# Kernel optimization log

Measured on AMD Instinct MI355X. Metric: run time of the kernel, lower is better.

The kernel has to match this reference:

```python
import jax, jax.numpy as jnp
import numpy as np

B, N, D_MODEL, N_HEADS, WINDOW = 2, 2048, 1024, 16, 512
HEAD_DIM = D_MODEL // N_HEADS

def setup_inputs() -> dict:
    key = jax.random.key(0)
    k1, k2, k3 = jax.random.split(key, 3)
    x = jax.random.normal(k1, (B, N, D_MODEL), dtype=jnp.float32)
    W_qkv = jax.random.normal(k2, (D_MODEL, 3 * D_MODEL), dtype=jnp.float32) * 0.02
    W_proj = jax.random.normal(k3, (D_MODEL, D_MODEL), dtype=jnp.float32) * 0.02
    b_proj = jnp.zeros((D_MODEL,), dtype=jnp.float32)
    return {"x": x, "W_qkv": W_qkv, "W_proj": W_proj, "b_proj": b_proj}

def reference(x, W_qkv, W_proj, b_proj):
    Bx, Nx, C = x.shape
    H, Dh = N_HEADS, C // N_HEADS
    scale = Dh ** -0.5
    window = min(WINDOW, Nx)
    half = window // 2
    # qkv: [B,N,3C] -> [3,B,H,N,Dh]
    qkv = (x @ W_qkv).reshape(Bx, Nx, 3, H, Dh).transpose(2, 0, 3, 1, 4)
    q, k, v = qkv[0], qkv[1], qkv[2]
    # banded mask: allowed iff i-half <= j <= i+half
    i = jnp.arange(Nx)[:, None]
    j = jnp.arange(Nx)[None, :]
    allowed = jnp.abs(i - j) <= half  # [N,N] bool
    attn = jnp.einsum('bhqd,bhkd->bhqk', q, k) * scale
    attn = jnp.where(allowed[None, None], attn, -jnp.inf)
    attn = jax.nn.softmax(attn, axis=-1)
    out = jnp.einsum('bhqk,bhkd->bhqd', attn, v)
    out = out.transpose(0, 2, 1, 3).reshape(Bx, Nx, C)
    return out @ W_proj + b_proj
```

## Files before the change

kernel.cpp:

```cpp
#include <hip/hip_runtime.h>
#include <stdint.h>


typedef _Float16 f16x8 __attribute__((ext_vector_type(8)));
typedef _Float16 f16x4 __attribute__((ext_vector_type(4)));
typedef __fp16   fp16x2n __attribute__((ext_vector_type(2)));
typedef float    f32x2 __attribute__((ext_vector_type(2)));
typedef float    f32x4 __attribute__((ext_vector_type(4)));
typedef float    f32x16 __attribute__((ext_vector_type(16)));

#define MFMA16(a, b, c) __builtin_amdgcn_mfma_f32_16x16x32_f16((a), (b), (c), 0, 0, 0)
#define MFMA32(a, b, c) __builtin_amdgcn_mfma_f32_32x32x16_f16((a), (b), (c), 0, 0, 0)

__device__ __forceinline__ void gload16(const void* g, void* l) {
  __builtin_amdgcn_global_load_lds(
      (const __attribute__((address_space(1))) void*)g,
      (__attribute__((address_space(3))) void*)l, 16, 0, 0);
}

__device__ __forceinline__ unsigned pk2(float a, float b) {
  fp16x2n t = __builtin_amdgcn_cvt_pkrtz(a, b);
  return __builtin_bit_cast(unsigned, t);
}

__global__ __launch_bounds__(256) void prep(const float* __restrict__ x,
                                            const float* __restrict__ wqkv,
                                            const float* __restrict__ wproj,
                                            _Float16* __restrict__ Xb,
                                            _Float16* __restrict__ Wqt,
                                            _Float16* __restrict__ Wpt) {
  __shared__ float t[64][65];
  const int id = blockIdx.x, tid = threadIdx.x;
  if (id < 4096) {
    int i = (id * 256 + tid) * 4;
    float4 v = *(const float4*)(x + i);
    f16x4 h;
    h[0] = (_Float16)v.x; h[1] = (_Float16)v.y;
    h[2] = (_Float16)v.z; h[3] = (_Float16)v.w;
    *(f16x4*)(Xb + i) = h;
    return;
  }
  const float* in; _Float16* out; int N, bx, by;
  if (id < 4864) { int tt = id - 4096; in = wqkv; out = Wqt; N = 3072; bx = tt % 48; by = tt / 48; }
  else           { int tt = id - 4864; in = wproj; out = Wpt; N = 1024; bx = tt & 15; by = tt >> 4; }
  const int n0 = bx * 64, k0 = by * 64;
  {
    int j = tid & 63;
#pragma unroll
    for (int p = 0; p < 16; p++) {
      int i = p * 4 + (tid >> 6);
      t[i][j] = in[(size_t)(k0 + i) * N + n0 + j];
    }
  }
  __syncthreads();
  {
    int i = tid & 63;
#pragma unroll
    for (int p = 0; p < 16; p++) {
      int j = p * 4 + (tid >> 6);
      out[(size_t)(n0 + j) * 1024 + k0 + i] = (_Float16)t[i][j];
    }
  }
}

__global__ __launch_bounds__(256) void vtrans(const _Float16* __restrict__ V,
                                              _Float16* __restrict__ Vt) {
  __shared__ _Float16 t[64][66];
  const int tid = threadIdx.x;
  const int bh = blockIdx.y, n0 = blockIdx.x * 64;
  const _Float16* Vg = V + (size_t)bh * 131072;
  {
    int dh0 = (tid & 7) * 8;
#pragma unroll
    for (int p = 0; p < 2; p++) {
      int nl = p * 32 + (tid >> 3);
      f16x8 v = *(const f16x8*)(Vg + (size_t)(n0 + nl) * 64 + dh0);
#pragma unroll
      for (int e = 0; e < 8; e++) t[nl][dh0 + e] = v[e];
    }
  }
  __syncthreads();
  {
    int dh = tid >> 2, nb = (tid & 3) * 16;
    f16x8 a, b;
#pragma unroll
    for (int e = 0; e < 8; e++) { a[e] = t[nb + e][dh]; b[e] = t[nb + 8 + e][dh]; }
    _Float16* dst = Vt + (size_t)bh * 131072 + (size_t)dh * 2048 + n0 + nb;
    *(f16x8*)dst = a;
    *(f16x8*)(dst + 8) = b;
  }
}

template <int BM, int BN, int EPI>
__global__ __launch_bounds__(256) void gemm16(const _Float16* __restrict__ A,
                                              const _Float16* __restrict__ Bt,
                                              const int K,
                                              _Float16* __restrict__ oh,
                                              float* __restrict__ of,
                                              const float* __restrict__ bias,
                                              const int Nout) {
  constexpr int RF = BM / 32, CF = BN / 32;
  constexpr int SLABS = (BM + BN) / 8;
  __shared__ __align__(16) char smem[(BM + BN) * 128];
  char* As = smem;
  char* Bs = smem + BM * 128;
  const int tid = threadIdx.x, wave = tid >> 6, lane = tid & 63;
  const int il = lane & 15, ih = lane >> 4;
  const int bm = blockIdx.y * BM, bn = blockIdx.x * BN;
  const int wm = wave >> 1, wn = wave & 1;
  const int rs = lane >> 3, cp = lane & 7;

  f32x4 acc[RF][CF] = {};

  for (int k0 = 0; k0 < K; k0 += 64) {
    __syncthreads();
#pragma unroll
    for (int s0 = 0; s0 < SLABS / 4; s0++) {
      int s = wave + s0 * 4;
      int row = s * 8 + rs;
      int c = cp ^ (row & 7);
      if (row < BM)
        gload16(A + (size_t)(bm + row) * K + k0 + c * 8, As + s * 1024);
      else
        gload16(Bt + (size_t)(bn + row - BM) * K + k0 + c * 8, smem + s * 1024);
    }
    __syncthreads();
#pragma unroll
    for (int ks = 0; ks < 2; ks++) {
      f16x8 af[RF], bf[CF];
#pragma unroll
      for (int rf = 0; rf < RF; rf++) {
        int R = wm * (BM / 2) + rf * 16 + il;
        af[rf] = *(const f16x8*)(As + R * 128 + (((ks * 4 + ih) ^ (R & 7)) * 16));
      }
#pragma unroll
      for (int cf = 0; cf < CF; cf++) {
        int C = wn * (BN / 2) + cf * 16 + il;
        bf[cf] = *(const f16x8*)(Bs + C * 128 + (((ks * 4 + ih) ^ (C & 7)) * 16));
      }
#pragma unroll
      for (int rf = 0; rf < RF; rf++)
#pragma unroll
        for (int cf = 0; cf < CF; cf++)
          acc[rf][cf] = MFMA16(af[rf], bf[cf], acc[rf][cf]);
    }
  }

#pragma unroll
  for (int rf = 0; rf < RF; rf++)
#pragma unroll
    for (int cf = 0; cf < CF; cf++)
#pragma unroll
      for (int r = 0; r < 4; r++) {
        int row = bm + wm * (BM / 2) + rf * 16 + ih * 4 + r;
        int col = bn + wn * (BN / 2) + cf * 16 + il;
        float v = acc[rf][cf][r];
        if (EPI == 0) {
          int sec = col >> 10, cc = col & 1023;
          if (sec == 0) v *= 0.18033688f;
          size_t plane = (size_t)(sec * 32 + (row >> 11) * 16 + (cc >> 6));
          oh[plane * 131072 + (size_t)(row & 2047) * 64 + (cc & 63)] = (_Float16)v;
        } else {
          of[(size_t)row * Nout + col] = v + bias[col];
        }
      }
}

__global__ __launch_bounds__(512) void attn(const _Float16* __restrict__ QKV,
                                            const _Float16* __restrict__ VT,
                                            _Float16* __restrict__ O2) {
  __shared__ __align__(16) char smem[51200];
  const int tid = threadIdx.x, wave = tid >> 6, lane = tid & 63;
  const int qw = wave >> 1, sh = wave & 1;
  const int cl = lane & 31, hl = lane >> 5;
  const int rs = lane >> 3, cp = lane & 7;
  const int q0 = blockIdx.x * 128, bh = blockIdx.y;
  const _Float16* Qg = QKV + (size_t)bh * 131072;
  const _Float16* Kg = QKV + 4194304 + (size_t)bh * 131072;
  const _Float16* Vg = VT + (size_t)bh * 131072;
  const int t0 = (q0 >= 256) ? q0 - 256 : 0;
  const int t1 = (q0 + 384 <= 2048) ? q0 + 384 : 2048;
  const int niter = (t1 - t0) >> 6;

#pragma unroll
  for (int q = 0; q < 2; q++) {
    int s = 2 * wave + q;
    int row = s * 8 + rs;
    int c = cp ^ (row & 7);
    gload16(Qg + (size_t)(q0 + row) * 64 + c * 8, smem + s * 1024);
  }
  {
    char* B0 = smem + 18432;
    int row = wave * 8 + rs;
    int c = cp ^ (row & 7);
    gload16(Kg + (size_t)(t0 + row) * 64 + c * 8, B0 + wave * 1024);
    gload16(Vg + (size_t)row * 2048 + t0 + c * 8, B0 + 8192 + wave * 1024);
  }
  __syncthreads();

  f16x8 bq[4];
  {
    int row = 32 * qw + cl;
#pragma unroll
    for (int ks = 0; ks < 4; ks++)
      bq[ks] = *(const f16x8*)(smem + row * 128 + (((ks * 2 + hl) ^ (row & 7)) * 16));
  }
  __syncthreads();

  char* Pw = smem + wave * 2304;
  f32x16 oacc[2] = {};
  float l_acc = 0.f;
  const int a0 = q0 + 32 * qw;

  for (int i = 0; i < niter; i++) {
    const int kt = t0 + i * 64;
    char* Bc = smem + 18432 + (i & 1) * 16384;
    if (i + 1 < niter) {
      char* Bn = smem + 18432 + ((i + 1) & 1) * 16384;
      int row = wave * 8 + rs;
      int c = cp ^ (row & 7);
      gload16(Kg + (size_t)(kt + 64 + row) * 64 + c * 8, Bn + wave * 1024);
      gload16(Vg + (size_t)row * 2048 + (kt + 64) + c * 8, Bn + 8192 + wave * 1024);
    }
    const int d0 = a0 - (kt + 32 * sh);
    if (d0 < 288 && d0 > -288) {
      char* Ksm = Bc;
      char* Vsm = Bc + 8192;
      f32x16 st = {};
      {
        const int krow = 32 * sh + cl;
#pragma unroll
        for (int ks = 0; ks < 4; ks++) {
          f16x8 ak = *(const f16x8*)(Ksm + krow * 128 + (((ks * 2 + hl) ^ (krow & 7)) * 16));
          st = MFMA32(ak, bq[ks], st);
        }
      }
#pragma unroll
      for (int g = 0; g < 4; g++) {
        float v[4];
#pragma unroll
        for (int i2 = 0; i2 < 4; i2++) {
          float e = __builtin_amdgcn_exp2f(st[4 * g + i2]);
          int kl = 8 * g + 4 * hl + i2;
          if (d0 == 256) e = (cl <= kl) ? e : 0.f;
          else if (d0 == -256) e = (cl >= kl) ? e : 0.f;
          l_acc += e;
          v[i2] = e;
        }
        uint2 w2 = {pk2(v[0], v[1]), pk2(v[2], v[3])};
        *(uint2*)(Pw + cl * 72 + 16 * g + 8 * hl) = w2;
      }
#pragma unroll
      for (int ks2 = 0; ks2 < 2; ks2++) {
        union { uint2 u2[2]; f16x8 h; } bp;
        bp.u2[0] = *(const uint2*)(Pw + cl * 72 + 32 * ks2 + 16 * hl);
        bp.u2[1] = *(const uint2*)(Pw + cl * 72 + 32 * ks2 + 16 * hl + 8);
#pragma unroll
        for (int db = 0; db < 2; db++) {
          int vrow = 32 * db + cl;
          f16x8 av = *(const f16x8*)(Vsm + vrow * 128 +
                                     (((4 * sh + 2 * ks2 + hl) ^ (vrow & 7)) * 16));
          oacc[db] = MFMA32(av, bp.h, oacc[db]);
        }
      }
    }
    __syncthreads();
  }

  const float lp = l_acc + __shfl_xor(l_acc, 32);
  char* Mq = smem + qw * 8448;
  if (sh == 1) {
#pragma unroll
    for (int db = 0; db < 2; db++)
#pragma unroll
      for (int g = 0; g < 4; g++) {
        int dh0 = 32 * db + 8 * g + 4 * hl;
        f32x2 a = {oacc[db][4 * g + 0], oacc[db][4 * g + 1]};
        f32x2 b = {oacc[db][4 * g + 2], oacc[db][4 * g + 3]};
        *(f32x2*)(Mq + cl * 264 + dh0 * 4) = a;
        *(f32x2*)(Mq + cl * 264 + dh0 * 4 + 8) = b;
      }
    if (hl == 0) *(float*)(smem + 34816 + (qw * 32 + cl) * 4) = lp;
  }
  __syncthreads();
  if (sh == 0) {
    float lo = *(const float*)(smem + 34816 + (qw * 32 + cl) * 4);
    float inv = 1.0f / (lp + lo);
    const int b = bh >> 4, h = bh & 15;
    _Float16* dst = O2 + (size_t)(b * 2048 + a0 + cl) * 1024 + h * 64;
#pragma unroll
    for (int db = 0; db < 2; db++)
#pragma unroll
      for (int g = 0; g < 4; g++) {
        int dh0 = 32 * db + 8 * g + 4 * hl;
        f32x2 a = *(const f32x2*)(Mq + cl * 264 + dh0 * 4);
        f32x2 b2 = *(const f32x2*)(Mq + cl * 264 + dh0 * 4 + 8);
        uint2 pkd = {pk2((oacc[db][4 * g + 0] + a[0]) * inv,
                         (oacc[db][4 * g + 1] + a[1]) * inv),
                     pk2((oacc[db][4 * g + 2] + b2[0]) * inv,
                         (oacc[db][4 * g + 3] + b2[1]) * inv)};
        *(uint2*)(dst + dh0) = pkd;
      }
  }
}


extern "C" void kernel_launch(void* const* d_in, const int* in_sizes, int n_in,
                              void* d_out, int out_size, void* d_ws, size_t ws_size,
                              hipStream_t stream) {
  const float* x = (const float*)d_in[0];
  const float* wqkv = (const float*)d_in[1];
  const float* wproj = (const float*)d_in[2];
  const float* bproj = (const float*)d_in[3];
  float* out = (float*)d_out;
  char* ws = (char*)d_ws;

  _Float16* Xb  = (_Float16*)(ws);
  _Float16* Wqt = (_Float16*)(ws + (size_t)(8  << 20));
  _Float16* Wpt = (_Float16*)(ws + (size_t)(14 << 20));
  _Float16* QKV = (_Float16*)(ws + (size_t)(16 << 20));
  _Float16* Vt  = (_Float16*)(ws + (size_t)(40 << 20));
  _Float16* O2  = (_Float16*)(ws);

  prep<<<5120, 256, 0, stream>>>(x, wqkv, wproj, Xb, Wqt, Wpt);
  gemm16<128, 128, 0><<<dim3(24, 32), 256, 0, stream>>>(Xb, Wqt, 1024, QKV, nullptr,
                                                        nullptr, 0);
  vtrans<<<dim3(32, 32), 256, 0, stream>>>(QKV + 8388608, Vt);
  attn<<<dim3(16, 32), 512, 0, stream>>>(QKV, Vt, O2);
  gemm16<128, 64, 1><<<dim3(16, 32), 256, 0, stream>>>(O2, Wpt, 1024, nullptr, out,
                                                       bproj, 1024);
}
```

Baseline: 160.9 us.

## Double-buffer GEMM LDS tiles with K-step 32 to overlap loads and MFMA

The GEMM main loop now uses two LDS buffers with a K-step of 32 instead of one buffer with a K-step of 64. The next tile is prefetched via global_load_lds while MFMAs run on the current one, and the swizzle is adjusted to the 64-byte rows. This is meant to hide global load latency and cut the loop from two barriers per step to one, at the cost of twice as many iterations with less MFMA work between barriers. Total LDS footprint stays the same.

```diff
diff --git a/kernel.cpp b/kernel.cpp
--- a/kernel.cpp
+++ b/kernel.cpp
@@ -100,50 +100,63 @@
                                               const float* __restrict__ bias,
                                               const int Nout) {
   constexpr int RF = BM / 32, CF = BN / 32;
-  constexpr int SLABS = (BM + BN) / 8;
-  __shared__ __align__(16) char smem[(BM + BN) * 128];
-  char* As = smem;
-  char* Bs = smem + BM * 128;
+  constexpr int SLABS = (BM + BN) / 16;
+  constexpr int BUF = (BM + BN) * 64;
+  __shared__ __align__(16) char smem[2 * BUF];
   const int tid = threadIdx.x, wave = tid >> 6, lane = tid & 63;
   const int il = lane & 15, ih = lane >> 4;
   const int bm = blockIdx.y * BM, bn = blockIdx.x * BN;
   const int wm = wave >> 1, wn = wave & 1;
-  const int rs = lane >> 3, cp = lane & 7;
+  const int rsl = lane >> 2, cp4 = lane & 3;
 
   f32x4 acc[RF][CF] = {};
 
-  for (int k0 = 0; k0 < K; k0 += 64) {
+#pragma unroll
+  for (int s0 = 0; s0 < SLABS / 4; s0++) {
+    int s = wave + s0 * 4;
+    int row = s * 16 + rsl;
+    int c = cp4 ^ ((row >> 1) & 3);
+    if (row < BM)
+      gload16(A + (size_t)(bm + row) * K + c * 8, smem + s * 1024);
+    else
+      gload16(Bt + (size_t)(bn + row - BM) * K + c * 8, smem + s * 1024);
+  }
+  __syncthreads();
+
+  for (int k0 = 0; k0 < K; k0 += 32) {
+    char* Bc = smem + ((k0 >> 5) & 1) * BUF;
+    if (k0 + 32 < K) {
+      char* Bn = smem + (((k0 >> 5) + 1) & 1) * BUF;
+#pragma unroll
+      for (int s0 = 0; s0 < SLABS / 4; s0++) {
+        int s = wave + s0 * 4;
+        int row = s * 16 + rsl;
+        int c = cp4 ^ ((row >> 1) & 3);
+        if (row < BM)
+          gload16(A + (size_t)(bm + row) * K + k0 + 32 + c * 8, Bn + s * 1024);
+        else
+          gload16(Bt + (size_t)(bn + row - BM) * K + k0 + 32 + c * 8, Bn + s * 1024);
+      }
+    }
+    char* As = Bc;
+    char* Bs = Bc + BM * 64;
+    f16x8 af[RF], bf[CF];
+#pragma unroll
+    for (int rf = 0; rf < RF; rf++) {
+      int R = wm * (BM / 2) + rf * 16 + il;
+      af[rf] = *(const f16x8*)(As + R * 64 + ((ih ^ ((R >> 1) & 3)) * 16));
+    }
+#pragma unroll
+    for (int cf = 0; cf < CF; cf++) {
+      int C = wn * (BN / 2) + cf * 16 + il;
+      bf[cf] = *(const f16x8*)(Bs + C * 64 + ((ih ^ ((C >> 1) & 3)) * 16));
+    }
+#pragma unroll
+    for (int rf = 0; rf < RF; rf++)
+#pragma unroll
+      for (int cf = 0; cf < CF; cf++)
+        acc[rf][cf] = MFMA16(af[rf], bf[cf], acc[rf][cf]);
     __syncthreads();
-#pragma unroll
-    for (int s0 = 0; s0 < SLABS / 4; s0++) {
-      int s = wave + s0 * 4;
-      int row = s * 8 + rs;
-      int c = cp ^ (row & 7);
-      if (row < BM)
-        gload16(A + (size_t)(bm + row) * K + k0 + c * 8, As + s * 1024);
-      else
-        gload16(Bt + (size_t)(bn + row - BM) * K + k0 + c * 8, smem + s * 1024);
-    }
-    __syncthreads();
-#pragma unroll
-    for (int ks = 0; ks < 2; ks++) {
-      f16x8 af[RF], bf[CF];
-#pragma unroll
-      for (int rf = 0; rf < RF; rf++) {
-        int R = wm * (BM / 2) + rf * 16 + il;
-        af[rf] = *(const f16x8*)(As + R * 128 + (((ks * 4 + ih) ^ (R & 7)) * 16));
-      }
-#pragma unroll
-      for (int cf = 0; cf < CF; cf++) {
-        int C = wn * (BN / 2) + cf * 16 + il;
-        bf[cf] = *(const f16x8*)(Bs + C * 128 + (((ks * 4 + ih) ^ (C & 7)) * 16));
-      }
-#pragma unroll
-      for (int rf = 0; rf < RF; rf++)
-#pragma unroll
-        for (int cf = 0; cf < CF; cf++)
-          acc[rf][cf] = MFMA16(af[rf], bf[cf], acc[rf][cf]);
-    }
   }
 
 #pragma unroll
```

After: 164.9 us. 2.5% more time.
